# Kernel optimization log

Hardware: AMD Instinct MI355X
Metric: run time of the kernel (lower is better)

Reference implementation:

```python
import jax, jax.numpy as jnp
import numpy as np

N_NODES = 50000
N_EDGES = 1600000
F_IN = 32
F_OUT = 32


def setup_inputs() -> dict:
    key = jax.random.key(0)
    k1, k2, k3, k4, k5 = jax.random.split(key, 5)
    inputs = jax.random.normal(k1, (N_EDGES, F_IN), dtype=jnp.float32)
    src = jax.random.randint(k2, (N_EDGES,), 0, N_NODES, dtype=jnp.int32)
    dst = jax.random.randint(k3, (N_EDGES,), 0, N_NODES, dtype=jnp.int32)
    W = jax.random.normal(k4, (F_OUT, F_IN), dtype=jnp.float32) * (1.0 / np.sqrt(F_IN))
    b = jax.random.normal(k5, (F_OUT,), dtype=jnp.float32) * 0.01
    return {"inputs": inputs, "src": src, "dst": dst, "W": W, "b": b}


def reference(inputs, src, dst, W, b):
    # Step 1: node h = mean of incoming edge features (mean over in-edges).
    ones = jnp.ones((inputs.shape[0],), dtype=inputs.dtype)
    in_deg = jax.ops.segment_sum(ones, dst, num_segments=N_NODES)  # [N]
    node_sum = jax.ops.segment_sum(inputs, dst, num_segments=N_NODES)  # [N, F]
    node_mean = node_sum / jnp.maximum(in_deg, 1.0)[:, None]
    # Step 2: send_and_recv: msg = src node h; reduce = sum at dst node.
    node_h = jax.ops.segment_sum(node_mean[src], dst, num_segments=N_NODES)  # [N, F]
    # Step 3: edge h = mean of its two endpoint node features.
    edge_h = 0.5 * (node_h[src] + node_h[dst])  # [E, F]
    # Step 4: final linear projection on edge features.
    return edge_h @ W.T + b
```

## Files before the change

kernel.cpp:

```cpp
#include <hip/hip_runtime.h>

#define N_NODES 50000
#define N_EDGES 1600000
#define F 32
#define BSH 7
#define BSIZE (1 << BSH)
#define NB ((N_NODES + BSIZE - 1) >> BSH)
#define FILL_CHUNK 6144
#define EMASK 0x1FFFFF

typedef float f4 __attribute__((ext_vector_type(4)));
typedef _Float16 h4 __attribute__((ext_vector_type(4)));

__device__ __forceinline__ f4 nt_load4(const float* p) {
    return __builtin_nontemporal_load((const f4*)p);
}
__device__ __forceinline__ int nt_loadi(const int* p) {
    return __builtin_nontemporal_load(p);
}
__device__ __forceinline__ unsigned short nt_loadu16(const unsigned short* p) {
    return __builtin_nontemporal_load(p);
}

__global__ __launch_bounds__(256)
void k_bhist(const int* __restrict__ dst, int* __restrict__ bhist) {
    __shared__ int lh[NB];
    for (int i = threadIdx.x; i < NB; i += 256) lh[i] = 0;
    __syncthreads();
    for (int e = blockIdx.x * blockDim.x + threadIdx.x; e < N_EDGES;
         e += gridDim.x * blockDim.x)
        atomicAdd(&lh[dst[e] >> BSH], 1);
    __syncthreads();
    for (int i = threadIdx.x; i < NB; i += 256)
        if (lh[i]) atomicAdd(&bhist[i], lh[i]);
}

__global__ __launch_bounds__(512)
void k_bscan(const int* __restrict__ bhist,
             int* __restrict__ bucket_off,
             int* __restrict__ cursor) {
    __shared__ int s[512];
    int t = threadIdx.x;
    int v = (t < NB) ? bhist[t] : 0;
    s[t] = v;
    __syncthreads();
    for (int off = 1; off < 512; off <<= 1) {
        int u = (t >= off) ? s[t - off] : 0;
        __syncthreads();
        s[t] += u;
        __syncthreads();
    }
    if (t < NB) {
        int ex = s[t] - v;
        bucket_off[t] = ex;
        cursor[t] = ex;
    }
    if (t == NB - 1) bucket_off[NB] = s[t];
}

__global__ __launch_bounds__(256)
void k_coarse_fill(const int* __restrict__ dst,
                   const int* __restrict__ src,
                   int* __restrict__ cursor,
                   int* __restrict__ coarseE,
                   unsigned short* __restrict__ coarseS) {
    __shared__ int lh[NB];
    __shared__ int gb[NB];
    __shared__ unsigned int ds[FILL_CHUNK];
    int lo = blockIdx.x * FILL_CHUNK;
    int hi = min(lo + FILL_CHUNK, N_EDGES);
    int n_e = hi - lo;

    for (int i = threadIdx.x; i < NB; i += 256) lh[i] = 0;
    __syncthreads();
    for (int i = threadIdx.x; i < n_e; i += 256) {
        int d = dst[lo + i];
        ds[i] = ((unsigned)d << 16) | (unsigned)src[lo + i];
        atomicAdd(&lh[d >> BSH], 1);
    }
    __syncthreads();
    for (int i = threadIdx.x; i < NB; i += 256) {
        gb[i] = atomicAdd(&cursor[i], lh[i]);
        lh[i] = 0;
    }
    __syncthreads();
    for (int i = threadIdx.x; i < n_e; i += 256) {
        unsigned v = ds[i];
        int d = (int)(v >> 16);
        int bk = d >> BSH;
        int r = atomicAdd(&lh[bk], 1);
        int p = gb[bk] + r;
        coarseE[p] = (lo + i) | ((d & (BSIZE - 1)) << 21);
        coarseS[p] = (unsigned short)(v & 0xFFFFu);
    }
}

__global__ __launch_bounds__(256)
void k_exact_fill(const int* __restrict__ coarseE,
                  const unsigned short* __restrict__ coarseS,
                  const int* __restrict__ bucket_off,
                  int* __restrict__ row_off,
                  int* __restrict__ eid_sorted,
                  unsigned short* __restrict__ src_sorted) {
    __shared__ int cnt[BSIZE];
    __shared__ int s[BSIZE];
    __shared__ int cur[BSIZE];
    int tid = threadIdx.x;
    int b = blockIdx.x;
    int lo = bucket_off[b], hi = bucket_off[b + 1];

    if (tid < BSIZE) cnt[tid] = 0;
    __syncthreads();
    for (int i = lo + tid; i < hi; i += 256)
        atomicAdd(&cnt[(nt_loadi(&coarseE[i]) >> 21) & (BSIZE - 1)], 1);
    __syncthreads();
    if (tid < BSIZE) s[tid] = cnt[tid];
    __syncthreads();
    for (int off = 1; off < BSIZE; off <<= 1) {
        int v = 0;
        if (tid < BSIZE && tid >= off) v = s[tid - off];
        __syncthreads();
        if (tid < BSIZE) s[tid] += v;
        __syncthreads();
    }
    int nbase = b << BSH;
    if (tid < BSIZE) {
        int base = lo + s[tid] - cnt[tid];
        cur[tid] = base;
        if (nbase + tid < N_NODES) row_off[nbase + tid] = base;
    }
    if (b == NB - 1 && tid == 0) row_off[N_NODES] = N_EDGES;
    __syncthreads();
    for (int i = lo + tid; i < hi; i += 256) {
        int ev = nt_loadi(&coarseE[i]);
        int l = (ev >> 21) & (BSIZE - 1);
        int p = atomicAdd(&cur[l], 1);
        eid_sorted[p] = ev & EMASK;
        src_sorted[p] = nt_loadu16(&coarseS[i]);
    }
}

__global__ __launch_bounds__(256)
void k_node_mean(const float* __restrict__ inputs,
                 const int* __restrict__ eid_sorted,
                 const int* __restrict__ row_off,
                 _Float16* __restrict__ node_mean) {
    int wave = (blockIdx.x * blockDim.x + threadIdx.x) >> 6;
    if (wave >= N_NODES) return;
    int lane  = threadIdx.x & 63;
    int eslot = lane >> 3;
    int q     = lane & 7;

    int s0 = row_off[wave];
    int s1 = row_off[wave + 1];

    f4 acc = {0.f, 0.f, 0.f, 0.f};
    int i = s0 + eslot;
    int e = (i < s1) ? eid_sorted[i] : 0;
    while (i < s1) {
        int inext = i + 8;
        int enext = (inext < s1) ? eid_sorted[inext] : 0;
        f4 v = nt_load4(&inputs[(size_t)e * F + q * 4]);
        acc += v;
        i = inext; e = enext;
    }
    #pragma unroll
    for (int m = 8; m <= 32; m <<= 1) {
        acc.x += __shfl_xor(acc.x, m);
        acc.y += __shfl_xor(acc.y, m);
        acc.z += __shfl_xor(acc.z, m);
        acc.w += __shfl_xor(acc.w, m);
    }
    if (eslot == 0) {
        float r = 1.0f / fmaxf((float)(s1 - s0), 1.0f);
        f4 o = acc * r;
        *reinterpret_cast<h4*>(&node_mean[(size_t)wave * F + q * 4]) =
            __builtin_convertvector(o, h4);
    }
}

__global__ __launch_bounds__(256)
void k_node_h_project(const unsigned short* __restrict__ src_sorted,
                      const int* __restrict__ row_off,
                      const _Float16* __restrict__ node_mean,
                      const float* __restrict__ W,
                      _Float16* __restrict__ node_p) {
    __shared__ float Wl[32][33];
    __shared__ float hr[4][36];

    int tid = threadIdx.x;
    #pragma unroll
    for (int i = tid; i < 1024; i += 256) Wl[i >> 5][i & 31] = W[i];

    int wv    = tid >> 6;
    int lane  = tid & 63;
    int eslot = lane >> 3;
    int q     = lane & 7;
    int n     = blockIdx.x * 4 + wv;

    int s0 = row_off[n];
    int s1 = row_off[n + 1];

    f4 acc = {0.f, 0.f, 0.f, 0.f};
    int i = s0 + eslot;
    int s = (i < s1) ? (int)src_sorted[i] : 0;
    while (i < s1) {
        int inext = i + 8;
        int snext = (inext < s1) ? (int)src_sorted[inext] : 0;
        h4 v = *reinterpret_cast<const h4*>(&node_mean[(size_t)s * F + q * 4]);
        acc += __builtin_convertvector(v, f4);
        i = inext; s = snext;
    }
    #pragma unroll
    for (int m = 8; m <= 32; m <<= 1) {
        acc.x += __shfl_xor(acc.x, m);
        acc.y += __shfl_xor(acc.y, m);
        acc.z += __shfl_xor(acc.z, m);
        acc.w += __shfl_xor(acc.w, m);
    }
    if (eslot == 0) {
        *reinterpret_cast<f4*>(&hr[wv][q * 4]) = acc;
    }
    __syncthreads();

    if (tid < 128) {
        int ln = tid >> 5;
        int o  = tid & 31;
        float sacc = 0.f;
        #pragma unroll
        for (int i2 = 0; i2 < 32; ++i2) sacc += hr[ln][i2] * Wl[o][i2];
        node_p[(size_t)(blockIdx.x * 4 + ln) * F + o] = (_Float16)sacc;
    }
}

__global__ __launch_bounds__(256)
void k_edge_out(const int* __restrict__ src,
                const int* __restrict__ dst,
                const _Float16* __restrict__ node_p,
                const float* __restrict__ b,
                float* __restrict__ out) {
    int tid = blockIdx.x * blockDim.x + threadIdx.x;
    if (tid >= N_EDGES * 8) return;
    int e = tid >> 3;
    int q = tid & 7;
    int s = nt_loadi(&src[e]);
    int d = nt_loadi(&dst[e]);

    h4 ah = *reinterpret_cast<const h4*>(&node_p[(size_t)s * F + q * 4]);
    h4 ch = *reinterpret_cast<const h4*>(&node_p[(size_t)d * F + q * 4]);
    const f4 a  = __builtin_convertvector(ah, f4);
    const f4 c  = __builtin_convertvector(ch, f4);
    const f4 bb = *reinterpret_cast<const f4*>(&b[q * 4]);

    f4 r = 0.5f * (a + c) + bb;
    __builtin_nontemporal_store(r, (f4*)&out[(size_t)e * F + q * 4]);
}

extern "C" void kernel_launch(void* const* d_in, const int* in_sizes, int n_in,
                              void* d_out, int out_size, void* d_ws, size_t ws_size,
                              hipStream_t stream) {
    const float* inputs = (const float*)d_in[0];
    const int*   src    = (const int*)d_in[1];
    const int*   dst    = (const int*)d_in[2];
    const float* W      = (const float*)d_in[3];
    const float* b      = (const float*)d_in[4];
    float* out = (float*)d_out;

    int*  coarseE    = (int*)d_ws;
    int*  eid_sorted = coarseE + N_EDGES;
    int*  bhist      = eid_sorted + N_EDGES;
    int*  bucket_off = bhist + NB;
    int*  cursor     = bucket_off + NB + 1;
    int*  row_off    = cursor + NB;
    _Float16* node_mean = (_Float16*)(row_off + N_NODES + 1);
    _Float16* node_p    = node_mean + (size_t)N_NODES * F;
    unsigned short* coarseS    = (unsigned short*)(node_p + (size_t)N_NODES * F);
    unsigned short* src_sorted = coarseS + N_EDGES;

    hipMemsetAsync(bhist, 0, NB * sizeof(int), stream);

    k_bhist<<<512, 256, 0, stream>>>(dst, bhist);
    k_bscan<<<1, 512, 0, stream>>>(bhist, bucket_off, cursor);
    k_coarse_fill<<<(N_EDGES + FILL_CHUNK - 1) / FILL_CHUNK, 256, 0, stream>>>(
        dst, src, cursor, coarseE, coarseS);
    k_exact_fill<<<NB, 256, 0, stream>>>(
        coarseE, coarseS, bucket_off, row_off, eid_sorted, src_sorted);

    int node_blocks = (N_NODES + 3) / 4;
    k_node_mean<<<node_blocks, 256, 0, stream>>>(inputs, eid_sorted, row_off, node_mean);
    k_node_h_project<<<N_NODES / 4, 256, 0, stream>>>(
        src_sorted, row_off, node_mean, W, node_p);
    k_edge_out<<<(N_EDGES * 8 + 255) / 256, 256, 0, stream>>>(src, dst, node_p, b, out);
}
```

Measured before the change: 217.7 us.

## Fuse histogram with scan, batch nodes per projection block, widen edge gathers

Merges the bucket histogram and its prefix scan into one kernel, where the last-finishing block (tracked by an atomic counter) performs the scan, removing a launch. The node aggregation/projection kernel now handles 16 nodes per block using 8-wide half loads, amortizing W staging across more nodes. The edge output kernel uses a grid-stride loop with 8-element half gathers and two vector stores per thread, cutting thread count and index reloads. Adds threadfence/atomic overhead and lower per-node parallelism in the projection.

```diff
diff --git a/kernel.cpp b/kernel.cpp
--- a/kernel.cpp
+++ b/kernel.cpp
@@ -8,9 +8,14 @@
 #define NB ((N_NODES + BSIZE - 1) >> BSH)
 #define FILL_CHUNK 6144
 #define EMASK 0x1FFFFF
+#define BHIST_BLOCKS 512
+#define PNB 16
+#define EO_BLOCKS 4096
 
 typedef float f4 __attribute__((ext_vector_type(4)));
+typedef float f8 __attribute__((ext_vector_type(8)));
 typedef _Float16 h4 __attribute__((ext_vector_type(4)));
+typedef _Float16 h8 __attribute__((ext_vector_type(8)));
 
 __device__ __forceinline__ f4 nt_load4(const float* p) {
     return __builtin_nontemporal_load((const f4*)p);
@@ -23,8 +28,16 @@
 }
 
 __global__ __launch_bounds__(256)
-void k_bhist(const int* __restrict__ dst, int* __restrict__ bhist) {
+void k_bhist_scan(const int* __restrict__ dst,
+                  int* __restrict__ bhist,
+                  int* __restrict__ done_ctr,
+                  int* __restrict__ bucket_off,
+                  int* __restrict__ cursor) {
     __shared__ int lh[NB];
+    __shared__ int s[256];
+    __shared__ int cvals[2 * 256];
+    __shared__ int isLast;
+
     for (int i = threadIdx.x; i < NB; i += 256) lh[i] = 0;
     __syncthreads();
     for (int e = blockIdx.x * blockDim.x + threadIdx.x; e < N_EDGES;
@@ -33,29 +46,30 @@
     __syncthreads();
     for (int i = threadIdx.x; i < NB; i += 256)
         if (lh[i]) atomicAdd(&bhist[i], lh[i]);
-}
-
-__global__ __launch_bounds__(512)
-void k_bscan(const int* __restrict__ bhist,
-             int* __restrict__ bucket_off,
-             int* __restrict__ cursor) {
-    __shared__ int s[512];
+
+    __threadfence();
+    if (threadIdx.x == 0)
+        isLast = (atomicAdd(done_ctr, 1) == (int)gridDim.x - 1);
+    __syncthreads();
+    if (!isLast) return;
+
     int t = threadIdx.x;
-    int v = (t < NB) ? bhist[t] : 0;
-    s[t] = v;
-    __syncthreads();
-    for (int off = 1; off < 512; off <<= 1) {
+    int c0 = (2 * t     < NB) ? atomicAdd(&bhist[2 * t], 0)     : 0;
+    int c1 = (2 * t + 1 < NB) ? atomicAdd(&bhist[2 * t + 1], 0) : 0;
+    cvals[2 * t] = c0; cvals[2 * t + 1] = c1;
+    int sum = c0 + c1;
+    s[t] = sum;
+    __syncthreads();
+    for (int off = 1; off < 256; off <<= 1) {
         int u = (t >= off) ? s[t - off] : 0;
         __syncthreads();
         s[t] += u;
         __syncthreads();
     }
-    if (t < NB) {
-        int ex = s[t] - v;
-        bucket_off[t] = ex;
-        cursor[t] = ex;
-    }
-    if (t == NB - 1) bucket_off[NB] = s[t];
+    int ex = s[t] - sum;
+    if (2 * t < NB)     { bucket_off[2 * t] = ex;          cursor[2 * t] = ex; }
+    if (2 * t + 1 < NB) { bucket_off[2 * t + 1] = ex + c0; cursor[2 * t + 1] = ex + c0; }
+    if (t == 255) bucket_off[NB] = s[255];
 }
 
 __global__ __launch_bounds__(256)
@@ -186,50 +200,53 @@
                       const float* __restrict__ W,
                       _Float16* __restrict__ node_p) {
     __shared__ float Wl[32][33];
-    __shared__ float hr[4][36];
+    __shared__ float hr[PNB][36];
 
     int tid = threadIdx.x;
     #pragma unroll
     for (int i = tid; i < 1024; i += 256) Wl[i >> 5][i & 31] = W[i];
 
-    int wv    = tid >> 6;
-    int lane  = tid & 63;
-    int eslot = lane >> 3;
-    int q     = lane & 7;
-    int n     = blockIdx.x * 4 + wv;
-
-    int s0 = row_off[n];
-    int s1 = row_off[n + 1];
-
-    f4 acc = {0.f, 0.f, 0.f, 0.f};
-    int i = s0 + eslot;
-    int s = (i < s1) ? (int)src_sorted[i] : 0;
-    while (i < s1) {
-        int inext = i + 8;
-        int snext = (inext < s1) ? (int)src_sorted[inext] : 0;
-        h4 v = *reinterpret_cast<const h4*>(&node_mean[(size_t)s * F + q * 4]);
-        acc += __builtin_convertvector(v, f4);
-        i = inext; s = snext;
-    }
+    int wv  = tid >> 6;
+    int lane = tid & 63;
+    int es  = lane >> 2;
+    int q2  = lane & 3;
+    int nb0 = blockIdx.x * PNB;
+
     #pragma unroll
-    for (int m = 8; m <= 32; m <<= 1) {
-        acc.x += __shfl_xor(acc.x, m);
-        acc.y += __shfl_xor(acc.y, m);
-        acc.z += __shfl_xor(acc.z, m);
-        acc.w += __shfl_xor(acc.w, m);
-    }
-    if (eslot == 0) {
-        *reinterpret_cast<f4*>(&hr[wv][q * 4]) = acc;
-    }
-    __syncthreads();
-
-    if (tid < 128) {
-        int ln = tid >> 5;
-        int o  = tid & 31;
+    for (int k = 0; k < 4; ++k) {
+        int n = nb0 + wv * 4 + k;
+        int s0 = row_off[n], s1 = row_off[n + 1];
+        f8 acc = {0.f, 0.f, 0.f, 0.f, 0.f, 0.f, 0.f, 0.f};
+        int i = s0 + es;
+        int sN = (i < s1) ? (int)src_sorted[i] : 0;
+        while (i < s1) {
+            int inext = i + 16;
+            int snext = (inext < s1) ? (int)src_sorted[inext] : 0;
+            h8 v = *reinterpret_cast<const h8*>(&node_mean[(size_t)sN * F + q2 * 8]);
+            acc += __builtin_convertvector(v, f8);
+            i = inext; sN = snext;
+        }
+        #pragma unroll
+        for (int m = 4; m <= 32; m <<= 1) {
+            #pragma unroll
+            for (int j = 0; j < 8; ++j) acc[j] += __shfl_xor(acc[j], m);
+        }
+        if (es == 0) {
+            f4 lo4 = __builtin_shufflevector(acc, acc, 0, 1, 2, 3);
+            f4 hi4 = __builtin_shufflevector(acc, acc, 4, 5, 6, 7);
+            *reinterpret_cast<f4*>(&hr[wv * 4 + k][q2 * 8])     = lo4;
+            *reinterpret_cast<f4*>(&hr[wv * 4 + k][q2 * 8 + 4]) = hi4;
+        }
+    }
+    __syncthreads();
+
+    for (int idx = tid; idx < PNB * 32; idx += 256) {
+        int n = idx >> 5;
+        int o = idx & 31;
         float sacc = 0.f;
         #pragma unroll
-        for (int i2 = 0; i2 < 32; ++i2) sacc += hr[ln][i2] * Wl[o][i2];
-        node_p[(size_t)(blockIdx.x * 4 + ln) * F + o] = (_Float16)sacc;
+        for (int i2 = 0; i2 < 32; ++i2) sacc += hr[n][i2] * Wl[o][i2];
+        node_p[(size_t)(nb0 + n) * F + o] = (_Float16)sacc;
     }
 }
 
@@ -239,21 +256,27 @@
                 const _Float16* __restrict__ node_p,
                 const float* __restrict__ b,
                 float* __restrict__ out) {
-    int tid = blockIdx.x * blockDim.x + threadIdx.x;
-    if (tid >= N_EDGES * 8) return;
-    int e = tid >> 3;
-    int q = tid & 7;
-    int s = nt_loadi(&src[e]);
-    int d = nt_loadi(&dst[e]);
-
-    h4 ah = *reinterpret_cast<const h4*>(&node_p[(size_t)s * F + q * 4]);
-    h4 ch = *reinterpret_cast<const h4*>(&node_p[(size_t)d * F + q * 4]);
-    const f4 a  = __builtin_convertvector(ah, f4);
-    const f4 c  = __builtin_convertvector(ch, f4);
-    const f4 bb = *reinterpret_cast<const f4*>(&b[q * 4]);
-
-    f4 r = 0.5f * (a + c) + bb;
-    __builtin_nontemporal_store(r, (f4*)&out[(size_t)e * F + q * 4]);
+    int q2 = threadIdx.x & 3;
+    f4 bb0 = *reinterpret_cast<const f4*>(&b[q2 * 8]);
+    f4 bb1 = *reinterpret_cast<const f4*>(&b[q2 * 8 + 4]);
+    int stride = gridDim.x * blockDim.x;
+    for (int t = blockIdx.x * blockDim.x + threadIdx.x; t < N_EDGES * 4; t += stride) {
+        int e = t >> 2;
+        int s = nt_loadi(&src[e]);
+        int d = nt_loadi(&dst[e]);
+
+        h8 ah = *reinterpret_cast<const h8*>(&node_p[(size_t)s * F + q2 * 8]);
+        h8 ch = *reinterpret_cast<const h8*>(&node_p[(size_t)d * F + q2 * 8]);
+        f8 a = __builtin_convertvector(ah, f8);
+        f8 c = __builtin_convertvector(ch, f8);
+        f8 r = 0.5f * (a + c);
+
+        f4 r0 = __builtin_shufflevector(r, r, 0, 1, 2, 3) + bb0;
+        f4 r1 = __builtin_shufflevector(r, r, 4, 5, 6, 7) + bb1;
+        float* o = &out[(size_t)e * F + q2 * 8];
+        __builtin_nontemporal_store(r0, (f4*)o);
+        __builtin_nontemporal_store(r1, (f4*)(o + 4));
+    }
 }
 
 extern "C" void kernel_launch(void* const* d_in, const int* in_sizes, int n_in,
@@ -266,21 +289,22 @@
     const float* b      = (const float*)d_in[4];
     float* out = (float*)d_out;
 
-    int*  coarseE    = (int*)d_ws;
+    _Float16* node_mean = (_Float16*)d_ws;
+    _Float16* node_p    = node_mean + (size_t)N_NODES * F;
+    int*  coarseE    = (int*)(node_p + (size_t)N_NODES * F);
     int*  eid_sorted = coarseE + N_EDGES;
     int*  bhist      = eid_sorted + N_EDGES;
-    int*  bucket_off = bhist + NB;
+    int*  done_ctr   = bhist + NB;
+    int*  bucket_off = done_ctr + 1;
     int*  cursor     = bucket_off + NB + 1;
     int*  row_off    = cursor + NB;
-    _Float16* node_mean = (_Float16*)(row_off + N_NODES + 1);
-    _Float16* node_p    = node_mean + (size_t)N_NODES * F;
-    unsigned short* coarseS    = (unsigned short*)(node_p + (size_t)N_NODES * F);
+    unsigned short* coarseS    = (unsigned short*)(row_off + N_NODES + 1);
     unsigned short* src_sorted = coarseS + N_EDGES;
 
-    hipMemsetAsync(bhist, 0, NB * sizeof(int), stream);
-
-    k_bhist<<<512, 256, 0, stream>>>(dst, bhist);
-    k_bscan<<<1, 512, 0, stream>>>(bhist, bucket_off, cursor);
+    hipMemsetAsync(bhist, 0, (NB + 1) * sizeof(int), stream);
+
+    k_bhist_scan<<<BHIST_BLOCKS, 256, 0, stream>>>(
+        dst, bhist, done_ctr, bucket_off, cursor);
     k_coarse_fill<<<(N_EDGES + FILL_CHUNK - 1) / FILL_CHUNK, 256, 0, stream>>>(
         dst, src, cursor, coarseE, coarseS);
     k_exact_fill<<<NB, 256, 0, stream>>>(
@@ -288,7 +312,7 @@
 
     int node_blocks = (N_NODES + 3) / 4;
     k_node_mean<<<node_blocks, 256, 0, stream>>>(inputs, eid_sorted, row_off, node_mean);
-    k_node_h_project<<<N_NODES / 4, 256, 0, stream>>>(
+    k_node_h_project<<<N_NODES / PNB, 256, 0, stream>>>(
         src_sorted, row_off, node_mean, W, node_p);
-    k_edge_out<<<(N_EDGES * 8 + 255) / 256, 256, 0, stream>>>(src, dst, node_p, b, out);
-}
+    k_edge_out<<<EO_BLOCKS, 256, 0, stream>>>(src, dst, node_p, b, out);
+}
```

After: 253.7 us. +16.6%, slower.
